# Kernel tuning notes

Hardware: AMD Instinct MI355X
Metric: run time of the kernel (lower is better)

The kernel has to match this reference:

```python
import jax, jax.numpy as jnp
import numpy as np

MODEL_DIMS = 1024
NUM_LAYERS = 4
NUM_SUPPORT = 256


def setup_inputs() -> dict:
    key = jax.random.key(0)
    kx, kk, kv = jax.random.split(key, 3)
    x = jax.random.normal(kx, (4, 4096, MODEL_DIMS), dtype=jnp.float32)
    # Stacked per-layer parameters, matching nn.Parameter(torch.randn(...))
    keys = jax.random.normal(kk, (NUM_LAYERS, NUM_SUPPORT, MODEL_DIMS), dtype=jnp.float32)
    values = jax.random.normal(kv, (NUM_LAYERS, NUM_SUPPORT, MODEL_DIMS), dtype=jnp.float32)
    return {"x": x, "keys": keys, "values": values}


def reference(x, keys, values):
    # Chain of CleanUpKV layers: normalize -> scores -> softmax -> weighted values.
    def step(h, kv):
        k, v = kv  # k, v: [num_support, D]
        hn = h / (jnp.linalg.norm(h, axis=-1, keepdims=True) + 1e-9)
        scores = jnp.einsum('bsd,nd->bsn', hn, k)          # [B,S,num_support]
        w = jax.nn.softmax(scores, axis=-1)
        return jnp.einsum('bsn,nd->bsd', w, v), None

    out, _ = jax.lax.scan(step, x, (keys, values))
    return out
```

## Files before the change

kernel.cpp:

```cpp
#include <hip/hip_runtime.h>
#include <hip/hip_bf16.h>
#include <stdint.h>

#define D 1024
#define NSUP 256
#define ROWS 16384
#define MB 32
#define LTHREADS 512
#define LGRID (ROWS / MB)

typedef __attribute__((__ext_vector_type__(8))) __bf16 bf16x8;
typedef __attribute__((__ext_vector_type__(4))) float f32x4;

#define MFMA16(a, b, c) __builtin_amdgcn_mfma_f32_16x16x32_bf16((a), (b), (c), 0, 0, 0)

static __device__ __forceinline__ uint16_t bf16bits(float f) {
    __bf16 b = (__bf16)f;
    return *(uint16_t*)&b;
}

__global__ void cast_k_kernel(const float* __restrict__ K, __bf16* __restrict__ Kb) {
    int i = (blockIdx.x * 256 + threadIdx.x) * 4;
    float4 v = *(const float4*)(K + i);
    __bf16 o[4] __attribute__((aligned(8)));
    o[0] = (__bf16)v.x; o[1] = (__bf16)v.y; o[2] = (__bf16)v.z; o[3] = (__bf16)v.w;
    *(uint2*)(Kb + i) = *(const uint2*)o;
}

__global__ void transpose_v_kernel(const float* __restrict__ V, __bf16* __restrict__ Vt) {
    __shared__ __bf16 tile[64][72];
    int l = blockIdx.z;
    int d0 = blockIdx.x * 64, n0 = blockIdx.y * 64;
    const float* Vl = V + (size_t)l * NSUP * D;
    __bf16* Vtl = Vt + (size_t)l * D * NSUP;
    for (int j = 0; j < 16; ++j) {
        int idx = j * 256 + threadIdx.x;
        int n_l = idx >> 6, d_l = idx & 63;
        tile[d_l][n_l] = (__bf16)Vl[(size_t)(n0 + n_l) * D + d0 + d_l];
    }
    __syncthreads();
    for (int j = 0; j < 16; ++j) {
        int idx = j * 256 + threadIdx.x;
        int d_l = idx >> 6, n_l = idx & 63;
        Vtl[(size_t)(d0 + d_l) * NSUP + n0 + n_l] = tile[d_l][n_l];
    }
}

template<bool IN_F32, bool OUT_F32>
__global__ void __launch_bounds__(LTHREADS)
layer_kernel(const void* __restrict__ h_in, void* __restrict__ h_out,
             const __bf16* __restrict__ Kb, const __bf16* __restrict__ Vt,
             float* __restrict__ rnbuf) {
    __shared__ __align__(16) char pool[49152];
    __shared__ float red[MB][8];
    __shared__ float rnin[MB];
    char* wbuf = pool + 32768;

    const int tid = threadIdx.x;
    const int lane = tid & 63;
    const int wv = tid >> 6;
    const int llo = lane & 15, lhi = lane >> 4;
    const int swzk = (llo & 7) << 4;
    const int row0 = blockIdx.x * MB;

    if constexpr (IN_F32) {
        const float4* x4 = (const float4*)h_in;
        #pragma unroll
        for (int rr = 0; rr < 4; ++rr) {
            int row = wv * 4 + rr;
            const float4* p = x4 + (size_t)(row0 + row) * 256;
            float s = 0.f;
            #pragma unroll
            for (int j = 0; j < 4; ++j) {
                float4 v = p[j * 64 + lane];
                s += v.x * v.x + v.y * v.y + v.z * v.z + v.w * v.w;
            }
            #pragma unroll
            for (int off = 1; off < 64; off <<= 1) s += __shfl_xor(s, off);
            if (lane == 0) rnin[row] = 1.f / (sqrtf(s) + 1e-9f);
        }
        __syncthreads();
    } else {
        if (tid < MB) rnin[tid] = rnbuf[row0 + tid];
    }

    auto stage = [&](int dc) {
        char* buf = pool + (dc & 1) * 16384;
        if constexpr (IN_F32) {
            int srow = tid >> 4, c16 = tid & 15;
            int key = (srow & 7) << 4;
            const float4* p = (const float4*)((const float*)h_in
                              + (size_t)(row0 + srow) * D + dc * 256 + c16 * 16);
            float rn = rnin[srow];
            __bf16 t[16] __attribute__((aligned(16)));
            #pragma unroll
            for (int q = 0; q < 4; ++q) {
                float4 v = p[q];
                t[4 * q + 0] = (__bf16)(v.x * rn); t[4 * q + 1] = (__bf16)(v.y * rn);
                t[4 * q + 2] = (__bf16)(v.z * rn); t[4 * q + 3] = (__bf16)(v.w * rn);
            }
            int b0 = c16 * 32;
            *(bf16x8*)(buf + srow * 512 + (b0 ^ key))        = *(const bf16x8*)(t);
            *(bf16x8*)(buf + srow * 512 + ((b0 + 16) ^ key)) = *(const bf16x8*)(t + 8);
        } else {
            #pragma unroll
            for (int c = 0; c < 2; ++c) {
                int L = (c * 512 + tid) * 16;
                int row = L >> 9;
                int b = L & 511;
                const char* g = (const char*)h_in + (size_t)(row0 + row) * 2048 + dc * 512 + b;
                __builtin_amdgcn_global_load_lds(
                    (const __attribute__((address_space(1))) uint32_t*)g,
                    (__attribute__((address_space(3))) uint32_t*)(buf + L), 16, 0, 0);
            }
        }
    };

    f32x4 acc[2][2];
    #pragma unroll
    for (int rf = 0; rf < 2; ++rf)
        #pragma unroll
        for (int cf = 0; cf < 2; ++cf)
            acc[rf][cf] = (f32x4){0.f, 0.f, 0.f, 0.f};

    stage(0);
    __syncthreads();
    #pragma unroll 1
    for (int dc = 0; dc < 4; ++dc) {
        if (dc < 3) stage(dc + 1);
        const char* hb = pool + (dc & 1) * 16384;
        const __bf16* kb0 = Kb + (size_t)(wv * 32 + llo) * D + dc * 256 + lhi * 8;
        bf16x8 kbuf[2][2];
        #pragma unroll
        for (int cf = 0; cf < 2; ++cf)
            kbuf[0][cf] = *(const bf16x8*)(kb0 + (size_t)cf * 16 * D);
        #pragma unroll
        for (int kk = 0; kk < 8; ++kk) {
            if (kk < 7) {
                #pragma unroll
                for (int cf = 0; cf < 2; ++cf)
                    kbuf[(kk + 1) & 1][cf] = *(const bf16x8*)(kb0 + (size_t)cf * 16 * D + (kk + 1) * 32);
            }
            bf16x8 a0 = *(const bf16x8*)(hb + llo * 512 + ((kk * 64 + lhi * 16) ^ swzk));
            bf16x8 a1 = *(const bf16x8*)(hb + (16 + llo) * 512 + ((kk * 64 + lhi * 16) ^ swzk));
            #pragma unroll
            for (int cf = 0; cf < 2; ++cf) {
                acc[0][cf] = MFMA16(a0, kbuf[kk & 1][cf], acc[0][cf]);
                acc[1][cf] = MFMA16(a1, kbuf[kk & 1][cf], acc[1][cf]);
            }
        }
        __syncthreads();
    }

    float ee[2][2][4];
    #pragma unroll
    for (int rf = 0; rf < 2; ++rf)
        #pragma unroll
        for (int r = 0; r < 4; ++r) {
            int row = rf * 16 + lhi * 4 + r;
            float sc = (IN_F32 ? 1.f : rnin[row]) * 1.44269504f;
            float e0 = exp2f(acc[rf][0][r] * sc);
            float e1 = exp2f(acc[rf][1][r] * sc);
            ee[rf][0][r] = e0; ee[rf][1][r] = e1;
            float s = e0 + e1;
            s += __shfl_xor(s, 1); s += __shfl_xor(s, 2);
            s += __shfl_xor(s, 4); s += __shfl_xor(s, 8);
            if (llo == 0) red[row][wv] = s;
        }
    __syncthreads();
    #pragma unroll
    for (int rf = 0; rf < 2; ++rf)
        #pragma unroll
        for (int r = 0; r < 4; ++r) {
            int row = rf * 16 + lhi * 4 + r;
            const f32x4* rp = (const f32x4*)&red[row][0];
            f32x4 s0 = rp[0], s1 = rp[1];
            float S = (s0[0] + s0[1] + s0[2] + s0[3]) + (s1[0] + s1[1] + s1[2] + s1[3]);
            float inv = 1.f / S;
            #pragma unroll
            for (int cf = 0; cf < 2; ++cf) {
                int col = wv * 32 + cf * 16 + llo;
                *(__bf16*)(wbuf + row * 512 + ((col * 2) ^ ((row & 7) << 4))) =
                    (__bf16)(ee[rf][cf][r] * inv);
            }
        }
    __syncthreads();

    float sql[2][4];
    #pragma unroll
    for (int rf = 0; rf < 2; ++rf)
        #pragma unroll
        for (int r = 0; r < 4; ++r) sql[rf][r] = 0.f;

    #pragma unroll 1
    for (int ch = 0; ch < 4; ++ch) {
        f32x4 acc2[2][2];
        #pragma unroll
        for (int rf = 0; rf < 2; ++rf)
            #pragma unroll
            for (int c2 = 0; c2 < 2; ++c2)
                acc2[rf][c2] = (f32x4){0.f, 0.f, 0.f, 0.f};
        const __bf16* vt0 = Vt + (size_t)(wv * 128 + ch * 32 + llo) * NSUP + lhi * 8;
        bf16x8 vbuf[2][2];
        #pragma unroll
        for (int c2 = 0; c2 < 2; ++c2)
            vbuf[0][c2] = *(const bf16x8*)(vt0 + (size_t)c2 * 16 * NSUP);
        #pragma unroll
        for (int kk = 0; kk < 8; ++kk) {
            if (kk < 7) {
                #pragma unroll
                for (int c2 = 0; c2 < 2; ++c2)
                    vbuf[(kk + 1) & 1][c2] = *(const bf16x8*)(vt0 + (size_t)c2 * 16 * NSUP + (kk + 1) * 32);
            }
            bf16x8 a0 = *(const bf16x8*)(wbuf + llo * 512 + ((kk * 64 + lhi * 16) ^ swzk));
            bf16x8 a1 = *(const bf16x8*)(wbuf + (16 + llo) * 512 + ((kk * 64 + lhi * 16) ^ swzk));
            #pragma unroll
            for (int c2 = 0; c2 < 2; ++c2) {
                acc2[0][c2] = MFMA16(a0, vbuf[kk & 1][c2], acc2[0][c2]);
                acc2[1][c2] = MFMA16(a1, vbuf[kk & 1][c2], acc2[1][c2]);
            }
        }
        #pragma unroll
        for (int rf = 0; rf < 2; ++rf)
            #pragma unroll
            for (int c2 = 0; c2 < 2; ++c2)
                #pragma unroll
                for (int r = 0; r < 4; ++r) {
                    int row = rf * 16 + lhi * 4 + r;
                    int col = wv * 128 + ch * 32 + c2 * 16 + llo;
                    float v = acc2[rf][c2][r];
                    sql[rf][r] += v * v;
                    if constexpr (OUT_F32) {
                        ((float*)h_out)[(size_t)(row0 + row) * D + col] = v;
                    } else {
                        *(uint16_t*)((char*)h_out + (size_t)(row0 + row) * 2048
                                     + ((col * 2) ^ ((row & 7) << 4))) = bf16bits(v);
                    }
                }
    }

    if constexpr (!OUT_F32) {
        #pragma unroll
        for (int rf = 0; rf < 2; ++rf)
            #pragma unroll
            for (int r = 0; r < 4; ++r) {
                float s = sql[rf][r];
                s += __shfl_xor(s, 1); s += __shfl_xor(s, 2);
                s += __shfl_xor(s, 4); s += __shfl_xor(s, 8);
                if (llo == 0) red[rf * 16 + lhi * 4 + r][wv] = s;
            }
        __syncthreads();
        if (tid < MB) {
            const f32x4* rp = (const f32x4*)&red[tid][0];
            f32x4 s0 = rp[0], s1 = rp[1];
            float S = (s0[0] + s0[1] + s0[2] + s0[3]) + (s1[0] + s1[1] + s1[2] + s1[3]);
            rnbuf[row0 + tid] = 1.f / (sqrtf(S) + 1e-9f);
        }
    }
}

extern "C" void kernel_launch(void* const* d_in, const int* in_sizes, int n_in,
                              void* d_out, int out_size, void* d_ws, size_t ws_size,
                              hipStream_t stream) {
    const float* x = (const float*)d_in[0];
    const float* keys = (const float*)d_in[1];
    const float* values = (const float*)d_in[2];
    float* out = (float*)d_out;

    char* ws = (char*)d_ws;
    char*   h  = ws;
    __bf16* Kb = (__bf16*)(ws + 33554432);
    __bf16* Vt = (__bf16*)(ws + 35651584);
    float*  rn = (float*)(ws + 37748736);

    cast_k_kernel<<<1024, 256, 0, stream>>>(keys, Kb);
    transpose_v_kernel<<<dim3(16, 4, 4), 256, 0, stream>>>(values, Vt);

    const int LS = NSUP * D;
    layer_kernel<true,  false><<<LGRID, LTHREADS, 0, stream>>>(x, h, Kb,          Vt,          rn);
    layer_kernel<false, false><<<LGRID, LTHREADS, 0, stream>>>(h, h, Kb + LS,     Vt + LS,     rn);
    layer_kernel<false, false><<<LGRID, LTHREADS, 0, stream>>>(h, h, Kb + 2 * LS, Vt + 2 * LS, rn);
    layer_kernel<false, true ><<<LGRID, LTHREADS, 0, stream>>>(h, out, Kb + 3 * LS, Vt + 3 * LS, rn);
}
```

Baseline: 310.8 us.

## Prefetch whole K/V register fragments one chunk ahead with full unrolling

Replaces the per-k-step two-deep register prefetch of K and V fragments with full-chunk register double buffering. Each chunk's 16 fragments are loaded one chunk ahead, and the D and value-column loops are manually unrolled. The first V chunk is loaded before the softmax phase so its latency overlaps that work. This hides global/L2 load latency behind MFMAs, at the cost of a large increase in VGPR usage (64 extra bf16x8 registers), which may reduce occupancy. The stage lambda's LDS destination is also rewritten explicitly from dc.

New measurement: 321.9 us. 3.6% more time.

```diff
diff --git a/kernel.cpp b/kernel.cpp
--- a/kernel.cpp
+++ b/kernel.cpp
@@ -111,7 +111,7 @@
                 const char* g = (const char*)h_in + (size_t)(row0 + row) * 2048 + dc * 512 + b;
                 __builtin_amdgcn_global_load_lds(
                     (const __attribute__((address_space(1))) uint32_t*)g,
-                    (__attribute__((address_space(3))) uint32_t*)(buf + L), 16, 0, 0);
+                    (__attribute__((address_space(3))) uint32_t*)(pool + (dc & 1) * 16384 + L), 16, 0, 0);
             }
         }
     };
@@ -123,34 +123,53 @@
         for (int cf = 0; cf < 2; ++cf)
             acc[rf][cf] = (f32x4){0.f, 0.f, 0.f, 0.f};
 
-    stage(0);
-    __syncthreads();
-    #pragma unroll 1
-    for (int dc = 0; dc < 4; ++dc) {
+    const __bf16* kbase = Kb + (size_t)(wv * 32 + llo) * D + lhi * 8;
+    bf16x8 kfrA[16], kfrB[16];
+
+    auto loadK = [&](bf16x8 (&dst)[16], int dc) {
+        const __bf16* kn = kbase + dc * 256;
+        #pragma unroll
+        for (int cf = 0; cf < 2; ++cf)
+            #pragma unroll
+            for (int kk = 0; kk < 8; ++kk)
+                dst[cf * 8 + kk] = *(const bf16x8*)(kn + (size_t)cf * 16 * D + kk * 32);
+    };
+    auto runA = [&](int dc, bf16x8 (&cur)[16], bf16x8 (&nxt)[16], bool pre) {
         if (dc < 3) stage(dc + 1);
+        if (pre) loadK(nxt, dc + 1);
         const char* hb = pool + (dc & 1) * 16384;
-        const __bf16* kb0 = Kb + (size_t)(wv * 32 + llo) * D + dc * 256 + lhi * 8;
-        bf16x8 kbuf[2][2];
-        #pragma unroll
-        for (int cf = 0; cf < 2; ++cf)
-            kbuf[0][cf] = *(const bf16x8*)(kb0 + (size_t)cf * 16 * D);
         #pragma unroll
         for (int kk = 0; kk < 8; ++kk) {
-            if (kk < 7) {
-                #pragma unroll
-                for (int cf = 0; cf < 2; ++cf)
-                    kbuf[(kk + 1) & 1][cf] = *(const bf16x8*)(kb0 + (size_t)cf * 16 * D + (kk + 1) * 32);
-            }
             bf16x8 a0 = *(const bf16x8*)(hb + llo * 512 + ((kk * 64 + lhi * 16) ^ swzk));
             bf16x8 a1 = *(const bf16x8*)(hb + (16 + llo) * 512 + ((kk * 64 + lhi * 16) ^ swzk));
             #pragma unroll
             for (int cf = 0; cf < 2; ++cf) {
-                acc[0][cf] = MFMA16(a0, kbuf[kk & 1][cf], acc[0][cf]);
-                acc[1][cf] = MFMA16(a1, kbuf[kk & 1][cf], acc[1][cf]);
+                acc[0][cf] = MFMA16(a0, cur[cf * 8 + kk], acc[0][cf]);
+                acc[1][cf] = MFMA16(a1, cur[cf * 8 + kk], acc[1][cf]);
             }
         }
         __syncthreads();
-    }
+    };
+
+    stage(0);
+    loadK(kfrA, 0);
+    __syncthreads();
+    runA(0, kfrA, kfrB, true);
+    runA(1, kfrB, kfrA, true);
+    runA(2, kfrA, kfrB, true);
+    runA(3, kfrB, kfrA, false);
+
+    const __bf16* vbase = Vt + (size_t)(wv * 128 + llo) * NSUP + lhi * 8;
+    bf16x8 vfrA[16], vfrB[16];
+    auto loadV = [&](bf16x8 (&dst)[16], int ch) {
+        const __bf16* vn = vbase + (size_t)(ch * 32) * NSUP;
+        #pragma unroll
+        for (int c2 = 0; c2 < 2; ++c2)
+            #pragma unroll
+            for (int kk = 0; kk < 8; ++kk)
+                dst[c2 * 8 + kk] = *(const bf16x8*)(vn + (size_t)c2 * 16 * NSUP + kk * 32);
+    };
+    loadV(vfrA, 0);
 
     float ee[2][2][4];
     #pragma unroll
@@ -192,32 +211,22 @@
         #pragma unroll
         for (int r = 0; r < 4; ++r) sql[rf][r] = 0.f;
 
-    #pragma unroll 1
-    for (int ch = 0; ch < 4; ++ch) {
+    auto runC = [&](int ch, bf16x8 (&cur)[16], bf16x8 (&nxt)[16], bool pre) {
+        if (pre) loadV(nxt, ch + 1);
         f32x4 acc2[2][2];
         #pragma unroll
         for (int rf = 0; rf < 2; ++rf)
             #pragma unroll
             for (int c2 = 0; c2 < 2; ++c2)
                 acc2[rf][c2] = (f32x4){0.f, 0.f, 0.f, 0.f};
-        const __bf16* vt0 = Vt + (size_t)(wv * 128 + ch * 32 + llo) * NSUP + lhi * 8;
-        bf16x8 vbuf[2][2];
-        #pragma unroll
-        for (int c2 = 0; c2 < 2; ++c2)
-            vbuf[0][c2] = *(const bf16x8*)(vt0 + (size_t)c2 * 16 * NSUP);
         #pragma unroll
         for (int kk = 0; kk < 8; ++kk) {
-            if (kk < 7) {
-                #pragma unroll
-                for (int c2 = 0; c2 < 2; ++c2)
-                    vbuf[(kk + 1) & 1][c2] = *(const bf16x8*)(vt0 + (size_t)c2 * 16 * NSUP + (kk + 1) * 32);
-            }
             bf16x8 a0 = *(const bf16x8*)(wbuf + llo * 512 + ((kk * 64 + lhi * 16) ^ swzk));
             bf16x8 a1 = *(const bf16x8*)(wbuf + (16 + llo) * 512 + ((kk * 64 + lhi * 16) ^ swzk));
             #pragma unroll
             for (int c2 = 0; c2 < 2; ++c2) {
-                acc2[0][c2] = MFMA16(a0, vbuf[kk & 1][c2], acc2[0][c2]);
-                acc2[1][c2] = MFMA16(a1, vbuf[kk & 1][c2], acc2[1][c2]);
+                acc2[0][c2] = MFMA16(a0, cur[c2 * 8 + kk], acc2[0][c2]);
+                acc2[1][c2] = MFMA16(a1, cur[c2 * 8 + kk], acc2[1][c2]);
             }
         }
         #pragma unroll
@@ -237,7 +246,11 @@
                                      + ((col * 2) ^ ((row & 7) << 4))) = bf16bits(v);
                     }
                 }
-    }
+    };
+    runC(0, vfrA, vfrB, true);
+    runC(1, vfrB, vfrA, true);
+    runC(2, vfrA, vfrB, true);
+    runC(3, vfrB, vfrA, false);
 
     if constexpr (!OUT_F32) {
         #pragma unroll
```

## Drop LDS staging of activations and transpose MFMA operands for vectorized stores

Applied to the files above, without the earlier changes.

The score GEMM no longer double-buffers activation tiles through shared memory. Each wave now loads its A-operand directly from global memory, with K as the first MFMA operand, so the score tile comes out transposed. Normalization is applied at the softmax step as a per-row scale. The value GEMM is reordered so each lane holds four consecutive output columns, which allows packed 8/16-byte output stores and unswizzled bf16 intermediate storage. This cuts LDS use and barriers, but every wave now reloads the same activation rows from global memory and the explicit K prefetch double-buffering is gone.

After: 441.0 us. 41.9% more time.

```diff
diff --git a/kernel.cpp b/kernel.cpp
--- a/kernel.cpp
+++ b/kernel.cpp
@@ -14,9 +14,9 @@
 
 #define MFMA16(a, b, c) __builtin_amdgcn_mfma_f32_16x16x32_bf16((a), (b), (c), 0, 0, 0)
 
-static __device__ __forceinline__ uint16_t bf16bits(float f) {
+static __device__ __forceinline__ uint32_t bfbits(float f) {
     __bf16 b = (__bf16)f;
-    return *(uint16_t*)&b;
+    return (uint32_t)*(uint16_t*)&b;
 }
 
 __global__ void cast_k_kernel(const float* __restrict__ K, __bf16* __restrict__ Kb) {
@@ -51,10 +51,9 @@
 layer_kernel(const void* __restrict__ h_in, void* __restrict__ h_out,
              const __bf16* __restrict__ Kb, const __bf16* __restrict__ Vt,
              float* __restrict__ rnbuf) {
-    __shared__ __align__(16) char pool[49152];
+    __shared__ __align__(16) char wtile[16384];
     __shared__ float red[MB][8];
     __shared__ float rnin[MB];
-    char* wbuf = pool + 32768;
 
     const int tid = threadIdx.x;
     const int lane = tid & 63;
@@ -63,6 +62,7 @@
     const int swzk = (llo & 7) << 4;
     const int row0 = blockIdx.x * MB;
 
+    float rnv[2];
     if constexpr (IN_F32) {
         const float4* x4 = (const float4*)h_in;
         #pragma unroll
@@ -80,175 +80,137 @@
             if (lane == 0) rnin[row] = 1.f / (sqrtf(s) + 1e-9f);
         }
         __syncthreads();
+        rnv[0] = rnin[llo];
+        rnv[1] = rnin[16 + llo];
     } else {
-        if (tid < MB) rnin[tid] = rnbuf[row0 + tid];
-    }
-
-    auto stage = [&](int dc) {
-        char* buf = pool + (dc & 1) * 16384;
-        if constexpr (IN_F32) {
-            int srow = tid >> 4, c16 = tid & 15;
-            int key = (srow & 7) << 4;
-            const float4* p = (const float4*)((const float*)h_in
-                              + (size_t)(row0 + srow) * D + dc * 256 + c16 * 16);
-            float rn = rnin[srow];
-            __bf16 t[16] __attribute__((aligned(16)));
-            #pragma unroll
-            for (int q = 0; q < 4; ++q) {
-                float4 v = p[q];
-                t[4 * q + 0] = (__bf16)(v.x * rn); t[4 * q + 1] = (__bf16)(v.y * rn);
-                t[4 * q + 2] = (__bf16)(v.z * rn); t[4 * q + 3] = (__bf16)(v.w * rn);
-            }
-            int b0 = c16 * 32;
-            *(bf16x8*)(buf + srow * 512 + (b0 ^ key))        = *(const bf16x8*)(t);
-            *(bf16x8*)(buf + srow * 512 + ((b0 + 16) ^ key)) = *(const bf16x8*)(t + 8);
-        } else {
-            #pragma unroll
-            for (int c = 0; c < 2; ++c) {
-                int L = (c * 512 + tid) * 16;
-                int row = L >> 9;
-                int b = L & 511;
-                const char* g = (const char*)h_in + (size_t)(row0 + row) * 2048 + dc * 512 + b;
-                __builtin_amdgcn_global_load_lds(
-                    (const __attribute__((address_space(1))) uint32_t*)g,
-                    (__attribute__((address_space(3))) uint32_t*)(buf + L), 16, 0, 0);
-            }
-        }
-    };
+        rnv[0] = rnbuf[row0 + llo];
+        rnv[1] = rnbuf[row0 + 16 + llo];
+    }
 
     f32x4 acc[2][2];
     #pragma unroll
-    for (int rf = 0; rf < 2; ++rf)
-        #pragma unroll
-        for (int cf = 0; cf < 2; ++cf)
-            acc[rf][cf] = (f32x4){0.f, 0.f, 0.f, 0.f};
-
-    stage(0);
-    __syncthreads();
-    #pragma unroll 1
-    for (int dc = 0; dc < 4; ++dc) {
-        if (dc < 3) stage(dc + 1);
-        const char* hb = pool + (dc & 1) * 16384;
-        const __bf16* kb0 = Kb + (size_t)(wv * 32 + llo) * D + dc * 256 + lhi * 8;
-        bf16x8 kbuf[2][2];
-        #pragma unroll
-        for (int cf = 0; cf < 2; ++cf)
-            kbuf[0][cf] = *(const bf16x8*)(kb0 + (size_t)cf * 16 * D);
-        #pragma unroll
-        for (int kk = 0; kk < 8; ++kk) {
-            if (kk < 7) {
-                #pragma unroll
-                for (int cf = 0; cf < 2; ++cf)
-                    kbuf[(kk + 1) & 1][cf] = *(const bf16x8*)(kb0 + (size_t)cf * 16 * D + (kk + 1) * 32);
-            }
-            bf16x8 a0 = *(const bf16x8*)(hb + llo * 512 + ((kk * 64 + lhi * 16) ^ swzk));
-            bf16x8 a1 = *(const bf16x8*)(hb + (16 + llo) * 512 + ((kk * 64 + lhi * 16) ^ swzk));
-            #pragma unroll
-            for (int cf = 0; cf < 2; ++cf) {
-                acc[0][cf] = MFMA16(a0, kbuf[kk & 1][cf], acc[0][cf]);
-                acc[1][cf] = MFMA16(a1, kbuf[kk & 1][cf], acc[1][cf]);
-            }
-        }
-        __syncthreads();
+    for (int kg = 0; kg < 2; ++kg)
+        #pragma unroll
+        for (int hg = 0; hg < 2; ++hg)
+            acc[kg][hg] = (f32x4){0.f, 0.f, 0.f, 0.f};
+
+    const __bf16* kb0 = Kb + (size_t)(wv * 32 + llo) * D + lhi * 8;
+    #pragma unroll
+    for (int ks = 0; ks < 32; ++ks) {
+        bf16x8 ka0 = *(const bf16x8*)(kb0 + ks * 32);
+        bf16x8 ka1 = *(const bf16x8*)(kb0 + (size_t)16 * D + ks * 32);
+        bf16x8 ha[2];
+        #pragma unroll
+        for (int hg = 0; hg < 2; ++hg) {
+            if constexpr (IN_F32) {
+                const float* xr = (const float*)h_in + (size_t)(row0 + hg * 16 + llo) * D
+                                  + ks * 32 + lhi * 8;
+                float4 f0 = *(const float4*)(xr);
+                float4 f1 = *(const float4*)(xr + 4);
+                __bf16 t[8] __attribute__((aligned(16)));
+                t[0] = (__bf16)f0.x; t[1] = (__bf16)f0.y; t[2] = (__bf16)f0.z; t[3] = (__bf16)f0.w;
+                t[4] = (__bf16)f1.x; t[5] = (__bf16)f1.y; t[6] = (__bf16)f1.z; t[7] = (__bf16)f1.w;
+                ha[hg] = *(const bf16x8*)t;
+            } else {
+                ha[hg] = *(const bf16x8*)((const char*)h_in
+                          + (size_t)(row0 + hg * 16 + llo) * 2048 + ks * 64 + lhi * 16);
+            }
+        }
+        acc[0][0] = MFMA16(ka0, ha[0], acc[0][0]);
+        acc[0][1] = MFMA16(ka0, ha[1], acc[0][1]);
+        acc[1][0] = MFMA16(ka1, ha[0], acc[1][0]);
+        acc[1][1] = MFMA16(ka1, ha[1], acc[1][1]);
     }
 
     float ee[2][2][4];
-    #pragma unroll
-    for (int rf = 0; rf < 2; ++rf)
-        #pragma unroll
-        for (int r = 0; r < 4; ++r) {
-            int row = rf * 16 + lhi * 4 + r;
-            float sc = (IN_F32 ? 1.f : rnin[row]) * 1.44269504f;
-            float e0 = exp2f(acc[rf][0][r] * sc);
-            float e1 = exp2f(acc[rf][1][r] * sc);
-            ee[rf][0][r] = e0; ee[rf][1][r] = e1;
-            float s = e0 + e1;
-            s += __shfl_xor(s, 1); s += __shfl_xor(s, 2);
-            s += __shfl_xor(s, 4); s += __shfl_xor(s, 8);
-            if (llo == 0) red[row][wv] = s;
-        }
-    __syncthreads();
-    #pragma unroll
-    for (int rf = 0; rf < 2; ++rf)
-        #pragma unroll
-        for (int r = 0; r < 4; ++r) {
-            int row = rf * 16 + lhi * 4 + r;
-            const f32x4* rp = (const f32x4*)&red[row][0];
-            f32x4 s0 = rp[0], s1 = rp[1];
-            float S = (s0[0] + s0[1] + s0[2] + s0[3]) + (s1[0] + s1[1] + s1[2] + s1[3]);
-            float inv = 1.f / S;
-            #pragma unroll
-            for (int cf = 0; cf < 2; ++cf) {
-                int col = wv * 32 + cf * 16 + llo;
-                *(__bf16*)(wbuf + row * 512 + ((col * 2) ^ ((row & 7) << 4))) =
-                    (__bf16)(ee[rf][cf][r] * inv);
-            }
-        }
-    __syncthreads();
-
-    float sql[2][4];
-    #pragma unroll
-    for (int rf = 0; rf < 2; ++rf)
-        #pragma unroll
-        for (int r = 0; r < 4; ++r) sql[rf][r] = 0.f;
-
-    #pragma unroll 1
-    for (int ch = 0; ch < 4; ++ch) {
-        f32x4 acc2[2][2];
-        #pragma unroll
-        for (int rf = 0; rf < 2; ++rf)
-            #pragma unroll
-            for (int c2 = 0; c2 < 2; ++c2)
-                acc2[rf][c2] = (f32x4){0.f, 0.f, 0.f, 0.f};
-        const __bf16* vt0 = Vt + (size_t)(wv * 128 + ch * 32 + llo) * NSUP + lhi * 8;
-        bf16x8 vbuf[2][2];
-        #pragma unroll
-        for (int c2 = 0; c2 < 2; ++c2)
-            vbuf[0][c2] = *(const bf16x8*)(vt0 + (size_t)c2 * 16 * NSUP);
-        #pragma unroll
-        for (int kk = 0; kk < 8; ++kk) {
-            if (kk < 7) {
-                #pragma unroll
-                for (int c2 = 0; c2 < 2; ++c2)
-                    vbuf[(kk + 1) & 1][c2] = *(const bf16x8*)(vt0 + (size_t)c2 * 16 * NSUP + (kk + 1) * 32);
-            }
-            bf16x8 a0 = *(const bf16x8*)(wbuf + llo * 512 + ((kk * 64 + lhi * 16) ^ swzk));
-            bf16x8 a1 = *(const bf16x8*)(wbuf + (16 + llo) * 512 + ((kk * 64 + lhi * 16) ^ swzk));
-            #pragma unroll
-            for (int c2 = 0; c2 < 2; ++c2) {
-                acc2[0][c2] = MFMA16(a0, vbuf[kk & 1][c2], acc2[0][c2]);
-                acc2[1][c2] = MFMA16(a1, vbuf[kk & 1][c2], acc2[1][c2]);
-            }
-        }
-        #pragma unroll
-        for (int rf = 0; rf < 2; ++rf)
-            #pragma unroll
-            for (int c2 = 0; c2 < 2; ++c2)
-                #pragma unroll
-                for (int r = 0; r < 4; ++r) {
-                    int row = rf * 16 + lhi * 4 + r;
-                    int col = wv * 128 + ch * 32 + c2 * 16 + llo;
-                    float v = acc2[rf][c2][r];
-                    sql[rf][r] += v * v;
-                    if constexpr (OUT_F32) {
-                        ((float*)h_out)[(size_t)(row0 + row) * D + col] = v;
-                    } else {
-                        *(uint16_t*)((char*)h_out + (size_t)(row0 + row) * 2048
-                                     + ((col * 2) ^ ((row & 7) << 4))) = bf16bits(v);
-                    }
-                }
-    }
-
-    if constexpr (!OUT_F32) {
-        #pragma unroll
-        for (int rf = 0; rf < 2; ++rf)
+    float part[2] = {0.f, 0.f};
+    #pragma unroll
+    for (int kg = 0; kg < 2; ++kg)
+        #pragma unroll
+        for (int hg = 0; hg < 2; ++hg)
             #pragma unroll
             for (int r = 0; r < 4; ++r) {
-                float s = sql[rf][r];
-                s += __shfl_xor(s, 1); s += __shfl_xor(s, 2);
-                s += __shfl_xor(s, 4); s += __shfl_xor(s, 8);
-                if (llo == 0) red[rf * 16 + lhi * 4 + r][wv] = s;
-            }
+                float e = exp2f(acc[kg][hg][r] * rnv[hg] * 1.44269504f);
+                ee[kg][hg][r] = e;
+                part[hg] += e;
+            }
+    #pragma unroll
+    for (int hg = 0; hg < 2; ++hg) {
+        part[hg] += __shfl_xor(part[hg], 16);
+        part[hg] += __shfl_xor(part[hg], 32);
+    }
+    if (lhi == 0) {
+        red[llo][wv] = part[0];
+        red[16 + llo][wv] = part[1];
+    }
+    __syncthreads();
+    #pragma unroll
+    for (int hg = 0; hg < 2; ++hg) {
+        int row = hg * 16 + llo;
+        const f32x4* rp = (const f32x4*)&red[row][0];
+        f32x4 s0 = rp[0], s1 = rp[1];
+        float S = (s0[0] + s0[1] + s0[2] + s0[3]) + (s1[0] + s1[1] + s1[2] + s1[3]);
+        float inv = 1.f / S;
+        #pragma unroll
+        for (int kg = 0; kg < 2; ++kg) {
+            uint32_t p0 = bfbits(ee[kg][hg][0] * inv) | (bfbits(ee[kg][hg][1] * inv) << 16);
+            uint32_t p1 = bfbits(ee[kg][hg][2] * inv) | (bfbits(ee[kg][hg][3] * inv) << 16);
+            uint2 pk = {p0, p1};
+            int nb = (wv * 32 + kg * 16 + lhi * 4) * 2;
+            *(uint2*)(wtile + row * 512 + (nb ^ swzk)) = pk;
+        }
+    }
+    __syncthreads();
+
+    f32x4 acc2[8][2];
+    #pragma unroll
+    for (int dg = 0; dg < 8; ++dg)
+        #pragma unroll
+        for (int hg = 0; hg < 2; ++hg)
+            acc2[dg][hg] = (f32x4){0.f, 0.f, 0.f, 0.f};
+
+    const __bf16* vt0 = Vt + (size_t)(wv * 128 + llo) * NSUP + lhi * 8;
+    #pragma unroll
+    for (int ks = 0; ks < 8; ++ks) {
+        bf16x8 wa0 = *(const bf16x8*)(wtile + llo * 512 + ((ks * 64 + lhi * 16) ^ swzk));
+        bf16x8 wa1 = *(const bf16x8*)(wtile + (16 + llo) * 512 + ((ks * 64 + lhi * 16) ^ swzk));
+        #pragma unroll
+        for (int dg = 0; dg < 8; ++dg) {
+            bf16x8 va = *(const bf16x8*)(vt0 + (size_t)(dg * 16) * NSUP + ks * 32);
+            acc2[dg][0] = MFMA16(va, wa0, acc2[dg][0]);
+            acc2[dg][1] = MFMA16(va, wa1, acc2[dg][1]);
+        }
+    }
+
+    float sql[2] = {0.f, 0.f};
+    #pragma unroll
+    for (int dg = 0; dg < 8; ++dg)
+        #pragma unroll
+        for (int hg = 0; hg < 2; ++hg) {
+            f32x4 v = acc2[dg][hg];
+            sql[hg] += v[0] * v[0] + v[1] * v[1] + v[2] * v[2] + v[3] * v[3];
+            int row = row0 + hg * 16 + llo;
+            int dcol = wv * 128 + dg * 16 + lhi * 4;
+            if constexpr (OUT_F32) {
+                *(f32x4*)((float*)h_out + (size_t)row * D + dcol) = v;
+            } else {
+                uint2 pk = {bfbits(v[0]) | (bfbits(v[1]) << 16),
+                            bfbits(v[2]) | (bfbits(v[3]) << 16)};
+                *(uint2*)((char*)h_out + (size_t)row * 2048 + dcol * 2) = pk;
+            }
+        }
+
+    if constexpr (!OUT_F32) {
+        #pragma unroll
+        for (int hg = 0; hg < 2; ++hg) {
+            sql[hg] += __shfl_xor(sql[hg], 16);
+            sql[hg] += __shfl_xor(sql[hg], 32);
+        }
+        __syncthreads();
+        if (lhi == 0) {
+            red[llo][wv] = sql[0];
+            red[16 + llo][wv] = sql[1];
+        }
         __syncthreads();
         if (tid < MB) {
             const f32x4* rp = (const f32x4*)&red[tid][0];
```
